# Kernel tuning notes

Hardware: AMD Instinct MI355X
Metric: run time of the kernel (lower is better)

The kernel has to match this reference:

```python
import jax, jax.numpy as jnp
import numpy as np

SAMPLE_RATE = 48000
NUM_SAMPLES = 24000
BATCH = 1024
EPS = 1e-4  # guards division by near-zero time constants


def _linear_recurrence(a, b):
    """y[n] = a[n] * y[n-1] + b[n], y[-1] = 0.  a, b: [N, B].
    Parallel prefix via associative scan (the kernel-friendly form of the IIR)."""
    def combine(l, r):
        A1, B1 = l
        A2, B2 = r
        return A1 * A2, A2 * B1 + B2
    _, y = jax.lax.associative_scan(combine, (a, b), axis=0)
    return y


def one_pole_lowpass(x, coeff):
    # x: [N, B], coeff: [B] in (0, 1); y[n] = (1-a)*x[n] + a*y[n-1]
    a = jnp.broadcast_to(coeff[None, :], x.shape)
    b = (1.0 - coeff)[None, :] * x
    return _linear_recurrence(a, b)


def one_pole_highpass(x, coeff):
    # complementary one-pole: remove the lowpassed component
    return x - one_pole_lowpass(x, coeff)


def exponential_envelope(num_samples, attack, decay):
    # attack, decay: [B] time constants (seconds); returns [N, B]
    t = jnp.arange(num_samples, dtype=jnp.float32)[:, None] / SAMPLE_RATE  # [N, 1]
    return (1.0 - jnp.exp(-t / (attack + EPS))) * jnp.exp(-t / (decay + EPS))


def setup_inputs() -> dict:
    key = jax.random.key(0)
    k1, k2 = jax.random.split(key)
    parameters = jax.random.uniform(k1, (5, BATCH), dtype=jnp.float32)
    noise = jax.random.normal(k2, (NUM_SAMPLES,), dtype=jnp.float32)
    return {"parameters": parameters, "noise": noise}


def reference(parameters, noise):
    attack, decay, f_lp, f_hp, gain = parameters  # each [B]
    env = exponential_envelope(NUM_SAMPLES, attack, decay)           # [N, B]
    x = jnp.broadcast_to(noise[:, None], (NUM_SAMPLES, parameters.shape[1]))
    x = one_pole_lowpass(x, f_lp)                                    # [N, B]
    x = one_pole_highpass(x, f_hp)                                   # [N, B]
    return x * env * gain[None, :]                                   # [N, B]
```

## Files before the change

### kernel.cpp

```cpp
#include <hip/hip_runtime.h>
#include <math.h>


#define NSAMP   24000
#define NBATCH  1024
#define SPT     100
#define NGRP    240
#define CPT     2
#define TPB     256
#define NCOLG   (NBATCH/(TPB*CPT))
#define EPSF    1e-4f
#define DT      (1.0f/48000.0f)

__global__ __launch_bounds__(TPB) void kA_aggr(const float* __restrict__ par,
                                               const float* __restrict__ noise,
                                               float* __restrict__ gv1,
                                               float* __restrict__ gv2) {
    const int g    = blockIdx.x;
    const int col0 = blockIdx.y * (TPB * CPT) + threadIdx.x * CPT;
    const int n0   = g * SPT;

    float a1[CPT], c1[CPT], a2[CPT], c2[CPT], y1[CPT], y2[CPT];
#pragma unroll
    for (int k = 0; k < CPT; ++k) {
        const int b = col0 + k;
        a1[k] = par[2 * NBATCH + b];
        a2[k] = par[3 * NBATCH + b];
        const float g_ = par[4 * NBATCH + b];
        c1[k] = (1.0f - a1[k]) * g_;
        c2[k] = 1.0f - a2[k];
        y1[k] = 0.0f; y2[k] = 0.0f;
    }

#pragma unroll 4
    for (int i = 0; i < SPT; ++i) {
        const float x = noise[n0 + i];
#pragma unroll
        for (int k = 0; k < CPT; ++k) {
            y1[k] = a1[k] * y1[k] + c1[k] * x;
            y2[k] = a2[k] * y2[k] + c2[k] * y1[k];
        }
    }
    *reinterpret_cast<float2*>(&gv1[g * NBATCH + col0]) = make_float2(y1[0], y1[1]);
    *reinterpret_cast<float2*>(&gv2[g * NBATCH + col0]) = make_float2(y2[0], y2[1]);
}

__global__ __launch_bounds__(64) void kB_scan(const float* __restrict__ par,
                                              float* __restrict__ gv1,
                                              float* __restrict__ gv2) {
    const int b = blockIdx.x * 64 + threadIdx.x;
    const float a1 = par[2 * NBATCH + b];
    const float a2 = par[3 * NBATCH + b];
    const float c2 = 1.0f - a2;

    float u1 = 1.0f, u2 = 0.0f, u3 = 1.0f;
#pragma unroll 4
    for (int i = 0; i < SPT; ++i) {
        u1 = a1 * u1;
        u2 = a2 * u2 + c2 * u1;
        u3 = a2 * u3;
    }
    const float p1 = u1, mL = u2, p2 = u3;

    float s1 = 0.0f, s2 = 0.0f;
#pragma unroll 4
    for (int c = 0; c < NGRP; ++c) {
        const float v1 = gv1[c * NBATCH + b];
        const float v2 = gv2[c * NBATCH + b];
        gv1[c * NBATCH + b] = s1;
        gv2[c * NBATCH + b] = s2;
        const float w  = mL * s1 + v2;
        s1 = p1 * s1 + v1;
        s2 = p2 * s2 + w;
    }
}

__global__ __launch_bounds__(TPB) void kC_out(const float* __restrict__ par,
                                              const float* __restrict__ noise,
                                              const float* __restrict__ gv1,
                                              const float* __restrict__ gv2,
                                              float* __restrict__ out) {
    const int g    = blockIdx.x;
    const int col0 = blockIdx.y * (TPB * CPT) + threadIdx.x * CPT;
    const int n0   = g * SPT;

    float a1[CPT], c1[CPT], a2[CPT], c2[CPT], y1[CPT], y2[CPT];
    float ea[CPT], ra[CPT], ed[CPT], rd[CPT];
    const float t0 = (float)n0 * DT;

    const float2 e1 = *reinterpret_cast<const float2*>(&gv1[g * NBATCH + col0]);
    const float2 e2 = *reinterpret_cast<const float2*>(&gv2[g * NBATCH + col0]);
    y1[0] = e1.x; y1[1] = e1.y;
    y2[0] = e2.x; y2[1] = e2.y;

#pragma unroll
    for (int k = 0; k < CPT; ++k) {
        const int b = col0 + k;
        const float ia  = 1.0f / (par[b] + EPSF);
        const float idc = 1.0f / (par[NBATCH + b] + EPSF);
        a1[k] = par[2 * NBATCH + b];
        a2[k] = par[3 * NBATCH + b];
        const float g_ = par[4 * NBATCH + b];
        c1[k] = (1.0f - a1[k]) * g_;
        c2[k] = 1.0f - a2[k];
        ea[k] = expf(-t0 * ia);   ra[k] = expf(-DT * ia);
        ed[k] = expf(-t0 * idc);  rd[k] = expf(-DT * idc);
    }

    float2* op = reinterpret_cast<float2*>(out + (size_t)n0 * NBATCH + col0);
#pragma unroll 4
    for (int i = 0; i < SPT; ++i) {
        const float x = noise[n0 + i];
        float2 o;
#pragma unroll
        for (int k = 0; k < CPT; ++k) {
            y1[k] = a1[k] * y1[k] + c1[k] * x;
            y2[k] = a2[k] * y2[k] + c2[k] * y1[k];
            const float env = (1.0f - ea[k]) * ed[k];
            (&o.x)[k] = (y1[k] - y2[k]) * env;
            ea[k] *= ra[k];
            ed[k] *= rd[k];
        }
        *op = o;
        op += NBATCH / 2;
    }
}

extern "C" void kernel_launch(void* const* d_in, const int* in_sizes, int n_in,
                              void* d_out, int out_size, void* d_ws, size_t ws_size,
                              hipStream_t stream) {
    const float* par   = (const float*)d_in[0];
    const float* noise = (const float*)d_in[1];
    float* out = (float*)d_out;
    float* gv1 = (float*)d_ws;
    float* gv2 = gv1 + (size_t)NGRP * NBATCH;

    kA_aggr<<<dim3(NGRP, NCOLG), dim3(TPB), 0, stream>>>(par, noise, gv1, gv2);
    kB_scan<<<dim3(16), dim3(64), 0, stream>>>(par, gv1, gv2);
    kC_out <<<dim3(NGRP, NCOLG), dim3(TPB), 0, stream>>>(par, noise, gv1, gv2, out);
}
```

Measured before the change: 136.5 us.

## Shorten chunks, widen per-thread columns, and stage scan carries in LDS

Halves the samples per chunk (doubling the number of chunks) and gives each thread four columns with float4 loads and stores in the aggregate and output kernels. The carry-propagation kernel now uses 64 blocks instead of 16. Each block stages a 16-column slab of per-chunk partials into shared memory with coalesced loads, runs the serial scan from LDS, and writes the results back. This targets the latency-bound serial scan over global memory and the narrow stores. In exchange the serial scan gets twice as many steps, is run by only 16 lanes per block, and the workspace doubles.

```diff
diff --git a/kernel.cpp b/kernel.cpp
--- a/kernel.cpp
+++ b/kernel.cpp
@@ -4,11 +4,10 @@
 
 #define NSAMP   24000
 #define NBATCH  1024
-#define SPT     100
-#define NGRP    240
-#define CPT     2
+#define SPT     50
+#define NGRP    480
+#define CPT     4
 #define TPB     256
-#define NCOLG   (NBATCH/(TPB*CPT))
 #define EPSF    1e-4f
 #define DT      (1.0f/48000.0f)
 
@@ -17,22 +16,24 @@
                                                float* __restrict__ gv1,
                                                float* __restrict__ gv2) {
     const int g    = blockIdx.x;
-    const int col0 = blockIdx.y * (TPB * CPT) + threadIdx.x * CPT;
+    const int col0 = threadIdx.x * CPT;
     const int n0   = g * SPT;
+
+    const float4 flp = *reinterpret_cast<const float4*>(&par[2 * NBATCH + col0]);
+    const float4 fhp = *reinterpret_cast<const float4*>(&par[3 * NBATCH + col0]);
+    const float4 gn  = *reinterpret_cast<const float4*>(&par[4 * NBATCH + col0]);
 
     float a1[CPT], c1[CPT], a2[CPT], c2[CPT], y1[CPT], y2[CPT];
 #pragma unroll
     for (int k = 0; k < CPT; ++k) {
-        const int b = col0 + k;
-        a1[k] = par[2 * NBATCH + b];
-        a2[k] = par[3 * NBATCH + b];
-        const float g_ = par[4 * NBATCH + b];
-        c1[k] = (1.0f - a1[k]) * g_;
+        a1[k] = (&flp.x)[k];
+        a2[k] = (&fhp.x)[k];
+        c1[k] = (1.0f - a1[k]) * (&gn.x)[k];
         c2[k] = 1.0f - a2[k];
         y1[k] = 0.0f; y2[k] = 0.0f;
     }
 
-#pragma unroll 4
+#pragma unroll 10
     for (int i = 0; i < SPT; ++i) {
         const float x = noise[n0 + i];
 #pragma unroll
@@ -41,37 +42,60 @@
             y2[k] = a2[k] * y2[k] + c2[k] * y1[k];
         }
     }
-    *reinterpret_cast<float2*>(&gv1[g * NBATCH + col0]) = make_float2(y1[0], y1[1]);
-    *reinterpret_cast<float2*>(&gv2[g * NBATCH + col0]) = make_float2(y2[0], y2[1]);
+    *reinterpret_cast<float4*>(&gv1[g * NBATCH + col0]) = make_float4(y1[0], y1[1], y1[2], y1[3]);
+    *reinterpret_cast<float4*>(&gv2[g * NBATCH + col0]) = make_float4(y2[0], y2[1], y2[2], y2[3]);
 }
 
-__global__ __launch_bounds__(64) void kB_scan(const float* __restrict__ par,
-                                              float* __restrict__ gv1,
-                                              float* __restrict__ gv2) {
-    const int b = blockIdx.x * 64 + threadIdx.x;
-    const float a1 = par[2 * NBATCH + b];
-    const float a2 = par[3 * NBATCH + b];
-    const float c2 = 1.0f - a2;
+#define KB_COLS 16
+__global__ __launch_bounds__(256) void kB_scan(const float* __restrict__ par,
+                                               float* __restrict__ gv1,
+                                               float* __restrict__ gv2) {
+    __shared__ float l1[NGRP][KB_COLS];
+    __shared__ float l2[NGRP][KB_COLS];
+    const int col0 = blockIdx.x * KB_COLS;
+    const int j    = threadIdx.x & (KB_COLS - 1);
+    const int r0   = threadIdx.x >> 4;
 
-    float u1 = 1.0f, u2 = 0.0f, u3 = 1.0f;
-#pragma unroll 4
-    for (int i = 0; i < SPT; ++i) {
-        u1 = a1 * u1;
-        u2 = a2 * u2 + c2 * u1;
-        u3 = a2 * u3;
+#pragma unroll 5
+    for (int r = r0; r < NGRP; r += 16) {
+        l1[r][j] = gv1[r * NBATCH + col0 + j];
+        l2[r][j] = gv2[r * NBATCH + col0 + j];
     }
-    const float p1 = u1, mL = u2, p2 = u3;
+    __syncthreads();
 
-    float s1 = 0.0f, s2 = 0.0f;
-#pragma unroll 4
-    for (int c = 0; c < NGRP; ++c) {
-        const float v1 = gv1[c * NBATCH + b];
-        const float v2 = gv2[c * NBATCH + b];
-        gv1[c * NBATCH + b] = s1;
-        gv2[c * NBATCH + b] = s2;
-        const float w  = mL * s1 + v2;
-        s1 = p1 * s1 + v1;
-        s2 = p2 * s2 + w;
+    if (threadIdx.x < KB_COLS) {
+        const int b = col0 + j;
+        const float a1 = par[2 * NBATCH + b];
+        const float a2 = par[3 * NBATCH + b];
+        const float c2 = 1.0f - a2;
+
+        float u1 = 1.0f, u2 = 0.0f, u3 = 1.0f;
+#pragma unroll 10
+        for (int i = 0; i < SPT; ++i) {
+            u1 = a1 * u1;
+            u2 = a2 * u2 + c2 * u1;
+            u3 = a2 * u3;
+        }
+        const float p1 = u1, mL = u2, p2 = u3;
+
+        float s1 = 0.0f, s2 = 0.0f;
+#pragma unroll 8
+        for (int c = 0; c < NGRP; ++c) {
+            const float v1 = l1[c][j];
+            const float v2 = l2[c][j];
+            l1[c][j] = s1;
+            l2[c][j] = s2;
+            const float w  = mL * s1 + v2;
+            s1 = p1 * s1 + v1;
+            s2 = p2 * s2 + w;
+        }
+    }
+    __syncthreads();
+
+#pragma unroll 5
+    for (int r = r0; r < NGRP; r += 16) {
+        gv1[r * NBATCH + col0 + j] = l1[r][j];
+        gv2[r * NBATCH + col0 + j] = l2[r][j];
     }
 }
 
@@ -81,37 +105,40 @@
                                               const float* __restrict__ gv2,
                                               float* __restrict__ out) {
     const int g    = blockIdx.x;
-    const int col0 = blockIdx.y * (TPB * CPT) + threadIdx.x * CPT;
+    const int col0 = threadIdx.x * CPT;
     const int n0   = g * SPT;
+
+    const float4 att4 = *reinterpret_cast<const float4*>(&par[0 * NBATCH + col0]);
+    const float4 dec4 = *reinterpret_cast<const float4*>(&par[1 * NBATCH + col0]);
+    const float4 flp  = *reinterpret_cast<const float4*>(&par[2 * NBATCH + col0]);
+    const float4 fhp  = *reinterpret_cast<const float4*>(&par[3 * NBATCH + col0]);
+    const float4 gn   = *reinterpret_cast<const float4*>(&par[4 * NBATCH + col0]);
+    const float4 e1   = *reinterpret_cast<const float4*>(&gv1[g * NBATCH + col0]);
+    const float4 e2   = *reinterpret_cast<const float4*>(&gv2[g * NBATCH + col0]);
 
     float a1[CPT], c1[CPT], a2[CPT], c2[CPT], y1[CPT], y2[CPT];
     float ea[CPT], ra[CPT], ed[CPT], rd[CPT];
     const float t0 = (float)n0 * DT;
 
-    const float2 e1 = *reinterpret_cast<const float2*>(&gv1[g * NBATCH + col0]);
-    const float2 e2 = *reinterpret_cast<const float2*>(&gv2[g * NBATCH + col0]);
-    y1[0] = e1.x; y1[1] = e1.y;
-    y2[0] = e2.x; y2[1] = e2.y;
-
 #pragma unroll
     for (int k = 0; k < CPT; ++k) {
-        const int b = col0 + k;
-        const float ia  = 1.0f / (par[b] + EPSF);
-        const float idc = 1.0f / (par[NBATCH + b] + EPSF);
-        a1[k] = par[2 * NBATCH + b];
-        a2[k] = par[3 * NBATCH + b];
-        const float g_ = par[4 * NBATCH + b];
-        c1[k] = (1.0f - a1[k]) * g_;
+        const float ia  = 1.0f / ((&att4.x)[k] + EPSF);
+        const float idc = 1.0f / ((&dec4.x)[k] + EPSF);
+        a1[k] = (&flp.x)[k];
+        a2[k] = (&fhp.x)[k];
+        c1[k] = (1.0f - a1[k]) * (&gn.x)[k];
         c2[k] = 1.0f - a2[k];
         ea[k] = expf(-t0 * ia);   ra[k] = expf(-DT * ia);
         ed[k] = expf(-t0 * idc);  rd[k] = expf(-DT * idc);
+        y1[k] = (&e1.x)[k];
+        y2[k] = (&e2.x)[k];
     }
 
-    float2* op = reinterpret_cast<float2*>(out + (size_t)n0 * NBATCH + col0);
-#pragma unroll 4
+    float4* op = reinterpret_cast<float4*>(out + (size_t)n0 * NBATCH + col0);
+#pragma unroll 5
     for (int i = 0; i < SPT; ++i) {
         const float x = noise[n0 + i];
-        float2 o;
+        float4 o;
 #pragma unroll
         for (int k = 0; k < CPT; ++k) {
             y1[k] = a1[k] * y1[k] + c1[k] * x;
@@ -122,7 +149,7 @@
             ed[k] *= rd[k];
         }
         *op = o;
-        op += NBATCH / 2;
+        op += NBATCH / 4;
     }
 }
 
@@ -135,7 +162,7 @@
     float* gv1 = (float*)d_ws;
     float* gv2 = gv1 + (size_t)NGRP * NBATCH;
 
-    kA_aggr<<<dim3(NGRP, NCOLG), dim3(TPB), 0, stream>>>(par, noise, gv1, gv2);
-    kB_scan<<<dim3(16), dim3(64), 0, stream>>>(par, gv1, gv2);
-    kC_out <<<dim3(NGRP, NCOLG), dim3(TPB), 0, stream>>>(par, noise, gv1, gv2, out);
+    kA_aggr<<<dim3(NGRP), dim3(TPB), 0, stream>>>(par, noise, gv1, gv2);
+    kB_scan<<<dim3(NBATCH / KB_COLS), dim3(256), 0, stream>>>(par, gv1, gv2);
+    kC_out <<<dim3(NGRP), dim3(TPB), 0, stream>>>(par, noise, gv1, gv2, out);
 }
```

After: 128.2 us. -6.1%, faster.
